# Kernel optimization log

Hardware: AMD Instinct MI355X
Metric: run time of the kernel (lower is better)

## Reference

```python
import jax, jax.numpy as jnp
import numpy as np

NH, HD, MB = 32, 64, 16        # heads, head_dim, TTT mini-batch size
BASE_LR = 1.0
ROPE_THETA = 10000.0


def _ln(x, w, b, eps):
    mu = x.mean(-1, keepdims=True)
    var = ((x - mu) ** 2).mean(-1, keepdims=True)
    return (x - mu) / jnp.sqrt(var + eps) * w + b


def _rotate_half(x):
    x1, x2 = jnp.split(x, 2, axis=-1)
    return jnp.concatenate([-x2, x1], axis=-1)


def _ln_l2_bwd(x, target, g, b, eps=1e-6):
    # grad of ||LN(x)*g+b - target||^2 / 2 wrt x (fused, as in ttt-lm)
    D = x.shape[-1]
    mu = x.mean(-1, keepdims=True)
    var = ((x - mu) ** 2).mean(-1, keepdims=True)
    std = jnp.sqrt(var + eps)
    xh = (x - mu) / std
    gxh = (g * xh + b - target) * g
    return (D * gxh - gxh.sum(-1, keepdims=True) - xh * (gxh * xh).sum(-1, keepdims=True)) / (D * std)


def _ttt_forward(x, q_w, k_w, v_w, o_w, ttt_lr_w, ttt_lr_b, token_idx_off,
                 ttt_norm_w, ttt_norm_b, W1, b1, post_w, post_b):
    B, L, C = x.shape
    NM = L // MB
    XQ = (x @ q_w).reshape(B, L, NH, HD).transpose(0, 2, 1, 3)  # [B,NH,L,HD]
    XK = (x @ k_w).reshape(B, L, NH, HD).transpose(0, 2, 1, 3)
    XV = (x @ v_w).reshape(B, L, NH, HD).transpose(0, 2, 1, 3)
    # rotary embedding at position_ids % mini_batch_size
    pos = (jnp.arange(L) % MB).astype(jnp.float32)
    inv = 1.0 / (ROPE_THETA ** (jnp.arange(0, HD, 2, dtype=jnp.float32) / HD))
    fr = pos[:, None] * inv[None, :]
    emb = jnp.concatenate([fr, fr], axis=-1)           # [L,HD]
    cos, sin = jnp.cos(emb), jnp.sin(emb)
    XQ = XQ * cos + _rotate_half(XQ) * sin
    XK = XK * cos + _rotate_half(XK) * sin
    # learning-rate gate (eta)
    Xm = x.reshape(B, NM, MB, C)
    ttt_lr = jax.nn.sigmoid(jnp.einsum('bnkc,hdc->bhnkd', Xm, ttt_lr_w)
                            + ttt_lr_b.reshape(1, NH, 1, 1, 1))       # [B,NH,NM,MB,1]
    ttt_lr_eta = BASE_LR * ttt_lr.transpose(0, 1, 2, 4, 3) / HD       # [B,NH,NM,1,MB]
    tok = jnp.maximum(1.0 / jnp.arange(1, MB + 1, dtype=jnp.float32) + token_idx_off, 0.0)
    eta = tok.reshape(1, 1, 1, MB, 1) * ttt_lr_eta                    # [B,NH,NM,MB,MB]

    def tomb(t):  # [B,NH,L,HD] -> [NM,B,NH,MB,HD]
        return t.reshape(B, NH, NM, MB, HD).transpose(2, 0, 1, 3, 4)

    xs = (tomb(XQ), tomb(XK), tomb(XV), eta.transpose(2, 0, 1, 3, 4))
    lw = ttt_norm_w.reshape(1, NH, 1, HD)
    lb = ttt_norm_b.reshape(1, NH, 1, HD)
    tril = jnp.tril(jnp.ones((MB, MB), x.dtype))
    W1s = jnp.broadcast_to(W1, (B, NH, HD, HD)).astype(x.dtype)
    b1s = jnp.broadcast_to(b1, (B, NH, 1, HD)).astype(x.dtype)

    def step(carry, xs_t):
        W1c, b1c = carry
        xq, xk, xv, et = xs_t                      # [B,NH,MB,HD], et [B,NH,MB,MB]
        Z1 = xk @ W1c + b1c
        grad = _ln_l2_bwd(Z1, xv - xk, lw, lb)     # grad of per-head TTT loss wrt Z1
        Attn1 = jnp.tril(xq @ xk.transpose(0, 1, 3, 2))
        b1_bar = b1c - (et * tril) @ grad
        Z1_bar = xq @ W1c - (et * Attn1) @ grad + b1_bar
        last_eta = et[:, :, -1, :, None]           # [B,NH,MB,1]
        W1n = W1c - jnp.einsum('bhki,bhkj->bhij', last_eta * xk, grad)
        b1n = b1c - (last_eta * grad).sum(-2, keepdims=True)
        out = xq + _ln(Z1_bar, lw, lb, 1e-6)
        return (W1n, b1n), out

    _, outs = jax.lax.scan(step, (W1s, b1s), xs)   # outs: [NM,B,NH,MB,HD]
    y = outs.transpose(1, 0, 3, 2, 4).reshape(B, L, C)
    y = _ln(y, post_w, post_b, 1e-6)
    return y @ o_w


def setup_inputs() -> dict:
    key = jax.random.key(0)
    ks = jax.random.split(key, 16)
    B, L, C, DH = 4, 2048, 2048, 1024
    s = 0.02
    return {
        'enc_input': jax.random.normal(ks[0], (B, L, C), jnp.float32),
        'ln1_w': jnp.ones((C,), jnp.float32), 'ln1_b': jnp.zeros((C,), jnp.float32),
        'q_w': jax.random.normal(ks[1], (C, C), jnp.float32) * s,
        'k_w': jax.random.normal(ks[2], (C, C), jnp.float32) * s,
        'v_w': jax.random.normal(ks[3], (C, C), jnp.float32) * s,
        'o_w': jax.random.normal(ks[4], (C, C), jnp.float32) * s,
        'ttt_lr_w': jax.random.normal(ks[5], (NH, 1, C), jnp.float32) * s,
        'ttt_lr_b': jax.random.normal(ks[6], (NH,), jnp.float32) * s,
        'token_idx_off': jax.random.normal(ks[7], (MB,), jnp.float32) * 0.01,
        'ttt_norm_w': jnp.ones((NH, HD), jnp.float32),
        'ttt_norm_b': jnp.zeros((NH, HD), jnp.float32),
        'W1': jax.random.normal(ks[8], (NH, HD, HD), jnp.float32) * s,
        'b1': jnp.zeros((NH, 1, HD), jnp.float32),
        'post_w': jnp.ones((C,), jnp.float32), 'post_b': jnp.zeros((C,), jnp.float32),
        'ffn_ln_w': jnp.ones((C,), jnp.float32), 'ffn_ln_b': jnp.zeros((C,), jnp.float32),
        'w1f': jax.random.normal(ks[9], (C, DH), jnp.float32) * s,
        'b1f': jnp.zeros((DH,), jnp.float32),
        'w2f': jax.random.normal(ks[10], (DH, C), jnp.float32) * s,
        'b2f': jnp.zeros((C,), jnp.float32),
    }


def reference(enc_input, ln1_w, ln1_b, q_w, k_w, v_w, o_w, ttt_lr_w, ttt_lr_b,
              token_idx_off, ttt_norm_w, ttt_norm_b, W1, b1, post_w, post_b,
              ffn_ln_w, ffn_ln_b, w1f, b1f, w2f, b2f):
    # pre-LN (torch default eps=1e-5) + TTT linear block + residual
    x = _ln(enc_input, ln1_w, ln1_b, 1e-5)
    y = _ttt_forward(x, q_w, k_w, v_w, o_w, ttt_lr_w, ttt_lr_b, token_idx_off,
                     ttt_norm_w, ttt_norm_b, W1, b1, post_w, post_b)
    y = y + enc_input
    # position-wise FFN (pre-LN eps=1e-6) + residual; dropout = eval no-op
    z = _ln(y, ffn_ln_w, ffn_ln_b, 1e-6)
    z = jax.nn.relu(z @ w1f + b1f) @ w2f + b2f
    return z + y
```

## Files before the change

### kernel.cpp

```cpp
#include <hip/hip_runtime.h>

typedef unsigned short u16;
typedef __attribute__((ext_vector_type(8))) short short8;
typedef __attribute__((ext_vector_type(8))) unsigned short ushort8;
typedef __attribute__((ext_vector_type(4))) float f32x4;
typedef __attribute__((ext_vector_type(2))) float f32x2;
typedef __attribute__((ext_vector_type(2))) unsigned int uint2v;

#define DEV __device__ __forceinline__

DEV float bf2f(u16 u){ union{unsigned int i; float f;} v; v.i = ((unsigned int)u)<<16u; return v.f; }
DEV u16 f2bf(float f){ union{float f; unsigned int i;} v; v.f=f; unsigned int r = v.i + 0x7FFFu + ((v.i>>16)&1u); return (u16)(r>>16); }

DEV void gload16(const u16* g, u16* l){
  __builtin_amdgcn_global_load_lds((const __attribute__((address_space(1))) void*)g,
                                   (__attribute__((address_space(3))) void*)l, 16, 0, 0);
}

DEV float wsum(float v){
  v += __shfl_xor(v, 32, 64);
  v += __shfl_xor(v, 16, 64);
  v += __shfl_xor(v, 8, 64);
  v += __shfl_xor(v, 4, 64);
  v += __shfl_xor(v, 2, 64);
  v += __shfl_xor(v, 1, 64);
  return v;
}

#if __has_builtin(__builtin_amdgcn_permlane16_swap) && __has_builtin(__builtin_amdgcn_permlane32_swap)
DEV float qsum(float v){
  unsigned u = __float_as_uint(v);
  uint2v a = __builtin_amdgcn_permlane16_swap(u, u, false, false);
  float s = __uint_as_float(a[0]) + __uint_as_float(a[1]);
  unsigned u2 = __float_as_uint(s);
  uint2v bsw = __builtin_amdgcn_permlane32_swap(u2, u2, false, false);
  return __uint_as_float(bsw[0]) + __uint_as_float(bsw[1]);
}
#else
DEV float qsum(float v){
  v += __shfl_xor(v, 16, 64);
  v += __shfl_xor(v, 32, 64);
  return v;
}
#endif

DEV float swap32(float v){ return __shfl_xor(v, 32, 64); }

DEV float block_sum(float v, float* red){
  v = wsum(v);
  __syncthreads();
  if((threadIdx.x & 63u)==0) red[threadIdx.x>>6] = v;
  __syncthreads();
  return red[0]+red[1]+red[2]+red[3];
}

#define BARS() do{ asm volatile("s_waitcnt lgkmcnt(0)" ::: "memory"); \
  __builtin_amdgcn_s_barrier(); __builtin_amdgcn_sched_barrier(0); }while(0)

__global__ __launch_bounds__(256) void ln_row(
    const float* __restrict__ in, const float* __restrict__ w, const float* __restrict__ bb,
    float eps, u16* __restrict__ outb)
{
  __shared__ float red[4];
  const int row = blockIdx.x, t = threadIdx.x;
  const float* p = in + (size_t)row*2048 + t*8;
  f32x4 a = *(const f32x4*)p;
  f32x4 c = *(const f32x4*)(p+4);
  float s = a[0]+a[1]+a[2]+a[3]+c[0]+c[1]+c[2]+c[3];
  s = block_sum(s, red);
  float mu = s*(1.f/2048.f);
  float vs = 0.f;
  #pragma unroll
  for(int j=0;j<4;j++){ float d=a[j]-mu; vs += d*d; }
  #pragma unroll
  for(int j=0;j<4;j++){ float d=c[j]-mu; vs += d*d; }
  vs = block_sum(vs, red);
  float rstd = rsqrtf(vs*(1.f/2048.f) + eps);
  f32x4 w0 = *(const f32x4*)(w + t*8);
  f32x4 w1 = *(const f32x4*)(w + t*8 + 4);
  f32x4 b0 = *(const f32x4*)(bb + t*8);
  f32x4 b1 = *(const f32x4*)(bb + t*8 + 4);
  ushort8 o;
  #pragma unroll
  for(int j=0;j<4;j++) o[j]   = f2bf((a[j]-mu)*rstd*w0[j] + b0[j]);
  #pragma unroll
  for(int j=0;j<4;j++) o[j+4] = f2bf((c[j]-mu)*rstd*w1[j] + b1[j]);
  *(ushort8*)(outb + (size_t)row*2048 + t*8) = o;
}

__global__ __launch_bounds__(256) void transpose_cast(
    const float* __restrict__ src, u16* __restrict__ dst, int K, int N)
{
  __shared__ float tile[32][33];
  const int kb = blockIdx.x*32, nb = blockIdx.y*32;
  const int tx = threadIdx.x & 31, ty = threadIdx.x >> 5;
  #pragma unroll
  for(int i=0;i<4;i++){
    int k = ty + i*8;
    tile[k][tx] = src[(size_t)(kb+k)*N + nb + tx];
  }
  __syncthreads();
  #pragma unroll
  for(int i=0;i<4;i++){
    int nn = ty + i*8;
    dst[(size_t)(nb+nn)*K + kb + tx] = f2bf(tile[tx][nn]);
  }
}

__global__ __launch_bounds__(256) void cast_lrw(const float* __restrict__ lrw, u16* __restrict__ dst)
{
  int i = blockIdx.x*256 + threadIdx.x;
  if (i < 32*2048) dst[i] = f2bf(lrw[i]);
  else dst[i] = 0;
}

__global__ void rope_init(const float* __restrict__ tio, float* __restrict__ cosb,
                          float* __restrict__ sinb, float* __restrict__ tokb)
{
  int t = blockIdx.x*256 + threadIdx.x;
  if (t < 1024){
// ... 119 lines not shown
          size_t idx = (size_t)(row0+rr)*Nld + col;
          float v = acc[mi][ni][rr];
          if (EPI==1 || EPI==3) v += resid[idx];
          if (EPI==2 || EPI==3) v += bias[col];
          if (EPI==2){ v = fmaxf(v, 0.f); Cb[idx] = f2bf(v); }
          else if (EPI==4){ Cb[idx] = f2bf(v); }
          else C[idx] = v;
        }
      }
    }
  }
}

#define W1LD 72
#define XLD  72
#define GTLD 40
#define EKLD 40
#define EALD 40
#define TD2  68

__global__ __launch_bounds__(512, 1) void ttt_scan(
    const u16* __restrict__ XQKV,
    const float* __restrict__ ropec, const float* __restrict__ ropes,
    const float* __restrict__ tokp,
    const float* __restrict__ nw, const float* __restrict__ nb,
    const float* __restrict__ lrb,
    const float* __restrict__ W1i,
    const float* __restrict__ b1i,
    float* __restrict__ Y)
{
  const int blk = blockIdx.x, b = blk>>5, h = blk&31;
  const int t = threadIdx.x, lane = t&63, wv = t>>6;
  const int fr = lane&15, quad = lane>>4;
  const int i0 = wv*2, i1 = i0+1;

  __shared__ u16 W1bf[2][64*W1LD];
  __shared__ u16 xqbf[2][16*XLD];
  __shared__ u16 xkbf[2][16*XLD];
  __shared__ u16 exkT[2][64*EKLD];
  __shared__ u16 gradTbf[2][64*GTLD];
  __shared__ u16 etaA[2][16*EALD];
  __shared__ float tgT2[2][16*TD2];
  __shared__ float xqT2[2][16*TD2];
  __shared__ float b1s[64];
  __shared__ float lrs[2][16];

  const float lrbh = lrb[h];
  const float cc0 = ropec[i0*64 + lane], ss0 = ropes[i0*64 + lane];
  const float cc1 = ropec[i1*64 + lane], ss1 = ropes[i1*64 + lane];
  const float ct = tokp[15]*(1.f/64.f);
  const float sg = (lane<32)? -1.f : 1.f;

  f32x2 lwr[16];
  #pragma unroll
  for(int m=0;m<4;m++)
    #pragma unroll
    for(int r=0;r<4;r++){
      int d = m*16+quad*4+r;
      lwr[m*4+r] = (f32x2){nw[h*64+d], nb[h*64+d]};
    }
  float tki[4];
  #pragma unroll
  for(int r=0;r<4;r++) tki[r] = tokp[quad*4+r];

  f32x4 wf0, wf1, wf2, wf3;
  if (wv < 4){
    const float* wsrc = W1i + (size_t)h*4096;
    #pragma unroll
    for(int r=0;r<4;r++){
      int d = wv*16+quad*4+r;
      wf0[r] = wsrc[( 0+fr)*64 + d];
      wf1[r] = wsrc[(16+fr)*64 + d];
      wf2[r] = wsrc[(32+fr)*64 + d];
      wf3[r] = wsrc[(48+fr)*64 + d];
    }
    #pragma unroll
    for(int r=0;r<4;r++){
      int d = wv*16+quad*4+r;
      W1bf[0][d*W1LD +  0 + fr] = f2bf(wf0[r]);
      W1bf[0][d*W1LD + 16 + fr] = f2bf(wf1[r]);
      W1bf[0][d*W1LD + 32 + fr] = f2bf(wf2[r]);
      W1bf[0][d*W1LD + 48 + fr] = f2bf(wf3[r]);
    }
  }
  for(int i=t;i<64*24;i+=512){
    int rr=i/24, cp=16+i%24;
    gradTbf[0][rr*GTLD+cp]=0; gradTbf[1][rr*GTLD+cp]=0;
    exkT[0][rr*EKLD+cp]=0;    exkT[1][rr*EKLD+cp]=0;
  }
  for(int i=t;i<16*24;i+=512){
    int rr=i/24, cp=16+i%24;
    etaA[0][rr*EALD+cp]=0; etaA[1][rr*EALD+cp]=0;
  }
  if (t<64) b1s[t]=b1i[h*64+t];

  auto stage = [&](int bf, u16 Pq0,u16 Pk0,u16 Pv0,u16 Pl0,
                           u16 Pq1,u16 Pk1,u16 Pv1,u16 Pl1){
    float q0=bf2f(Pq0), k0=bf2f(Pk0), v0=bf2f(Pv0);
    float q1=bf2f(Pq1), k1=bf2f(Pk1), v1=bf2f(Pv1);
    float qr0 = q0*cc0 + sg*swap32(q0)*ss0;
    float kr0 = k0*cc0 + sg*swap32(k0)*ss0;
    float qr1 = q1*cc1 + sg*swap32(q1)*ss1;
    float kr1 = k1*cc1 + sg*swap32(k1)*ss1;
    float lr0 = 1.f/(1.f + expf(-(bf2f(Pl0) + lrbh)));
    float lr1 = 1.f/(1.f + expf(-(bf2f(Pl1) + lrbh)));
    xqbf[bf][i0*XLD+lane] = f2bf(qr0);
    xqbf[bf][i1*XLD+lane] = f2bf(qr1);
    xkbf[bf][i0*XLD+lane] = f2bf(kr0);
    xkbf[bf][i1*XLD+lane] = f2bf(kr1);
    exkT[bf][lane*EKLD+i0] = f2bf(-ct*lr0*kr0);
    exkT[bf][lane*EKLD+i1] = f2bf(-ct*lr1*kr1);
    tgT2[bf][i0*TD2+lane] = v0 - kr0;
    tgT2[bf][i1*TD2+lane] = v1 - kr1;
    xqT2[bf][i0*TD2+lane] = qr0;
    xqT2[bf][i1*TD2+lane] = qr1;
    if (lane==0){ lrs[bf][i0]=lr0; lrs[bf][i1]=lr1; }
  };

  {
    const size_t rb = (size_t)b*2048;
    const u16* p0 = XQKV + (rb+i0)*6272 + h*64 + lane;
    const u16* p1 = XQKV + (rb+i1)*6272 + h*64 + lane;
    u16 l0 = XQKV[(rb+i0)*6272 + 6144 + h];
    u16 l1 = XQKV[(rb+i1)*6272 + 6144 + h];
    stage(0, p0[0],p0[2048],p0[4096],l0, p1[0],p1[2048],p1[4096],l1);
  }
  __syncthreads();

  const f32x4 fzero = (f32x4){0.f,0.f,0.f,0.f};

  f32x4 zqP0=fzero, zqP1=fzero, zqP2=fzero, zqP3=fzero;
  f32x4 b1qP0=fzero, b1qP1=fzero, b1qP2=fzero, b1qP3=fzero;

  auto do_out = [&](int pbuf, size_t rb){
    short8 be = *(const short8*)&etaA[pbuf][fr*EALD + quad*8];
    f32x4 c20,c21,c22,c23;
    c20 = __builtin_amdgcn_mfma_f32_16x16x32_bf16(*(const short8*)&gradTbf[pbuf][( 0+fr)*GTLD + quad*8], be, fzero, 0,0,0);
    c21 = __builtin_amdgcn_mfma_f32_16x16x32_bf16(*(const short8*)&gradTbf[pbuf][(16+fr)*GTLD + quad*8], be, fzero, 0,0,0);
    c22 = __builtin_amdgcn_mfma_f32_16x16x32_bf16(*(const short8*)&gradTbf[pbuf][(32+fr)*GTLD + quad*8], be, fzero, 0,0,0);
    c23 = __builtin_amdgcn_mfma_f32_16x16x32_bf16(*(const short8*)&gradTbf[pbuf][(48+fr)*GTLD + quad*8], be, fzero, 0,0,0);
    f32x4 xqv0 = *(const f32x4*)&xqT2[pbuf][fr*TD2 +  0 + quad*4];
    f32x4 xqv1 = *(const f32x4*)&xqT2[pbuf][fr*TD2 + 16 + quad*4];
    f32x4 xqv2 = *(const f32x4*)&xqT2[pbuf][fr*TD2 + 32 + quad*4];
    f32x4 xqv3 = *(const f32x4*)&xqT2[pbuf][fr*TD2 + 48 + quad*4];
    f32x4 zb0,zb1,zb2,zb3;
    float s1=0.f, s2=0.f;
    #pragma unroll
    for(int r=0;r<4;r++){
      zb0[r] = zqP0[r] + b1qP0[r] + c20[r];
      zb1[r] = zqP1[r] + b1qP1[r] + c21[r];
      zb2[r] = zqP2[r] + b1qP2[r] + c22[r];
      zb3[r] = zqP3[r] + b1qP3[r] + c23[r];
      s1 += zb0[r]+zb1[r]+zb2[r]+zb3[r];
      s2 += zb0[r]*zb0[r]+zb1[r]*zb1[r]+zb2[r]*zb2[r]+zb3[r]*zb3[r];
    }
    s1 = qsum(s1); s2 = qsum(s2);
    float mu = s1*(1.f/64.f);
    float var = s2*(1.f/64.f) - mu*mu;
    float rstd = rsqrtf(var + 1e-6f);
    #pragma unroll
    for(int m=0;m<4;m++){
      f32x4* zp = (m==0)?&zb0:(m==1)?&zb1:(m==2)?&zb2:&zb3;
      const f32x4* xp = (m==0)?&xqv0:(m==1)?&xqv1:(m==2)?&xqv2:&xqv3;
      f32x4 o;
      #pragma unroll
      for(int r=0;r<4;r++){
        f32x2 wb = lwr[m*4+r];
        float xh = ((*zp)[r] - mu)*rstd;
        o[r] = (*xp)[r] + xh*wb[0] + wb[1];
      }
      *(f32x4*)&Y[(rb+fr)*2048 + h*64 + m*16 + quad*4] = o;
    }
  };

  for(int n=0;n<128;n++){
    const int cur = n&1, nxt = cur^1, pb = cur^1;
    const int cb = cur, nbuf = cur^1;
    const size_t rbase = (size_t)b*2048 + n*16;

    u16 Pq0=0,Pk0=0,Pv0=0,Pl0=0,Pq1=0,Pk1=0,Pv1=0,Pl1=0;
    if (n<127){
      const size_t rb2 = rbase + 16;
      const u16* p0 = XQKV + (rb2+i0)*6272 + h*64 + lane;
      const u16* p1 = XQKV + (rb2+i1)*6272 + h*64 + lane;
      Pq0=p0[0]; Pk0=p0[2048]; Pv0=p0[4096];
      Pq1=p1[0]; Pk1=p1[2048]; Pv1=p1[4096];
      Pl0=XQKV[(rb2+i0)*6272 + 6144 + h];
      Pl1=XQKV[(rb2+i1)*6272 + 6144 + h];
    }

    if (wv < 2){
      f32x4 b1v0 = *(const f32x4*)&b1s[ 0+quad*4];
      f32x4 b1v1 = *(const f32x4*)&b1s[16+quad*4];
      f32x4 b1v2 = *(const f32x4*)&b1s[32+quad*4];
      f32x4 b1v3 = *(const f32x4*)&b1s[48+quad*4];
      f32x4 tgv0 = *(const f32x4*)&tgT2[cur][fr*TD2 +  0 + quad*4];
      f32x4 tgv1 = *(const f32x4*)&tgT2[cur][fr*TD2 + 16 + quad*4];
      f32x4 tgv2 = *(const f32x4*)&tgT2[cur][fr*TD2 + 32 + quad*4];
      f32x4 tgv3 = *(const f32x4*)&tgT2[cur][fr*TD2 + 48 + quad*4];
      short8 bk0 = *(const short8*)&xkbf[cur][fr*XLD + quad*8];
      short8 bk1 = *(const short8*)&xkbf[cur][fr*XLD + 32 + quad*8];
      f32x4 z0,z1,z2,z3;
      z0 = __builtin_amdgcn_mfma_f32_16x16x32_bf16(*(const short8*)&W1bf[cb][( 0+fr)*W1LD + quad*8],      bk0, fzero, 0,0,0);
      z0 = __builtin_amdgcn_mfma_f32_16x16x32_bf16(*(const short8*)&W1bf[cb][( 0+fr)*W1LD + 32 + quad*8], bk1, z0,    0,0,0);
      z1 = __builtin_amdgcn_mfma_f32_16x16x32_bf16(*(const short8*)&W1bf[cb][(16+fr)*W1LD + quad*8],      bk0, fzero, 0,0,0);
      z1 = __builtin_amdgcn_mfma_f32_16x16x32_bf16(*(const short8*)&W1bf[cb][(16+fr)*W1LD + 32 + quad*8], bk1, z1,    0,0,0);
      z2 = __builtin_amdgcn_mfma_f32_16x16x32_bf16(*(const short8*)&W1bf[cb][(32+fr)*W1LD + quad*8],      bk0, fzero, 0,0,0);
      z2 = __builtin_amdgcn_mfma_f32_16x16x32_bf16(*(const short8*)&W1bf[cb][(32+fr)*W1LD + 32 + quad*8], bk1, z2,    0,0,0);
      z3 = __builtin_amdgcn_mfma_f32_16x16x32_bf16(*(const short8*)&W1bf[cb][(48+fr)*W1LD + quad*8],      bk0, fzero, 0,0,0);
      z3 = __builtin_amdgcn_mfma_f32_16x16x32_bf16(*(const short8*)&W1bf[cb][(48+fr)*W1LD + 32 + quad*8], bk1, z3,    0,0,0);
      f32x4 xh0,xh1,xh2,xh3;
      {
        float s1=0.f, s2=0.f;
        #pragma unroll
        for(int r=0;r<4;r++){
          z0[r] += b1v0[r];
          z1[r] += b1v1[r];
          z2[r] += b1v2[r];
          z3[r] += b1v3[r];
          s1 += z0[r]+z1[r]+z2[r]+z3[r];
          s2 += z0[r]*z0[r]+z1[r]*z1[r]+z2[r]*z2[r]+z3[r]*z3[r];
        }
        s1 = qsum(s1); s2 = qsum(s2);
        float mu = s1*(1.f/64.f);
        float var = s2*(1.f/64.f) - mu*mu;
        float rstd = rsqrtf(var + 1e-6f);
        float u1=0.f, u2=0.f;
        #pragma unroll
        for(int m=0;m<4;m++){
          f32x4* zp = (m==0)?&z0:(m==1)?&z1:(m==2)?&z2:&z3;
          f32x4* xp = (m==0)?&xh0:(m==1)?&xh1:(m==2)?&xh2:&xh3;
          const f32x4* tp = (m==0)?&tgv0:(m==1)?&tgv1:(m==2)?&tgv2:&tgv3;
          #pragma unroll
          for(int r=0;r<4;r++){
            f32x2 wb = lwr[m*4+r];
            float xh = ((*zp)[r] - mu)*rstd;
            float gx = (wb[0]*xh + wb[1] - (*tp)[r])*wb[0];
            (*xp)[r] = xh;
            (*zp)[r] = gx;
            u1 += gx; u2 += gx*xh;
          }
        }
        u1 = qsum(u1); u2 = qsum(u2);
        const float c64 = rstd*(1.f/64.f);
        #pragma unroll
        for(int m=0;m<4;m++){
          f32x4* zp = (m==0)?&z0:(m==1)?&z1:(m==2)?&z2:&z3;
          f32x4* xp = (m==0)?&xh0:(m==1)?&xh1:(m==2)?&xh2:&xh3;
          #pragma unroll
          for(int r=0;r<4;r++)
            (*zp)[r] = (64.f*(*zp)[r] - u1 - (*xp)[r]*u2)*c64;
        }
      }
      f32x4 zA = (wv==0)? z0 : z2;
      f32x4 zB = (wv==0)? z1 : z3;
      const int rb0 = wv*32;
      #pragma unroll
      for(int r=0;r<4;r++){
        gradTbf[cur][(rb0+quad*4+r)*GTLD + fr]    = f2bf(zA[r]);
        gradTbf[cur][(rb0+16+quad*4+r)*GTLD + fr] = f2bf(zB[r]);
      }
    }
    else if (wv == 4){
      short8 bq0 = *(const short8*)&xqbf[cur][fr*XLD + quad*8];
      short8 bq1 = *(const short8*)&xqbf[cur][fr*XLD + 32 + quad*8];
      f32x4 zqN0,zqN1,zqN2,zqN3;
      zqN0 = __builtin_amdgcn_mfma_f32_16x16x32_bf16(*(const short8*)&W1bf[cb][( 0+fr)*W1LD + quad*8],      bq0, fzero, 0,0,0);
      zqN0 = __builtin_amdgcn_mfma_f32_16x16x32_bf16(*(const short8*)&W1bf[cb][( 0+fr)*W1LD + 32 + quad*8], bq1, zqN0,  0,0,0);
      zqN1 = __builtin_amdgcn_mfma_f32_16x16x32_bf16(*(const short8*)&W1bf[cb][(16+fr)*W1LD + quad*8],      bq0, fzero, 0,0,0);
      zqN1 = __builtin_amdgcn_mfma_f32_16x16x32_bf16(*(const short8*)&W1bf[cb][(16+fr)*W1LD + 32 + quad*8], bq1, zqN1,  0,0,0);
      zqN2 = __builtin_amdgcn_mfma_f32_16x16x32_bf16(*(const short8*)&W1bf[cb][(32+fr)*W1LD + quad*8],      bq0, fzero, 0,0,0);
      zqN2 = __builtin_amdgcn_mfma_f32_16x16x32_bf16(*(const short8*)&W1bf[cb][(32+fr)*W1LD + 32 + quad*8], bq1, zqN2,  0,0,0);
      zqN3 = __builtin_amdgcn_mfma_f32_16x16x32_bf16(*(const short8*)&W1bf[cb][(48+fr)*W1LD + quad*8],      bq0, fzero, 0,0,0);
      zqN3 = __builtin_amdgcn_mfma_f32_16x16x32_bf16(*(const short8*)&W1bf[cb][(48+fr)*W1LD + 32 + quad*8], bq1, zqN3,  0,0,0);
      if (n > 0) do_out(pb, rbase - 16);
      zqP0=zqN0; zqP1=zqN1; zqP2=zqN2; zqP3=zqN3;
      b1qP0 = *(const f32x4*)&b1s[ 0+quad*4];
      b1qP1 = *(const f32x4*)&b1s[16+quad*4];
      b1qP2 = *(const f32x4*)&b1s[32+quad*4];
      b1qP3 = *(const f32x4*)&b1s[48+quad*4];
    }
    else if (wv == 7){
      short8 aq0 = *(const short8*)&xqbf[cur][fr*XLD + quad*8];
      short8 aq1 = *(const short8*)&xqbf[cur][fr*XLD + 32 + quad*8];
      short8 bk0 = *(const short8*)&xkbf[cur][fr*XLD + quad*8];
      short8 bk1 = *(const short8*)&xkbf[cur][fr*XLD + 32 + quad*8];
      f32x4 at;
      at = __builtin_amdgcn_mfma_f32_16x16x32_bf16(aq0, bk0, fzero, 0,0,0);
      at = __builtin_amdgcn_mfma_f32_16x16x32_bf16(aq1, bk1, at,    0,0,0);
      float lrj = lrs[cur][fr]*(1.f/64.f);
      #pragma unroll
      for(int r=0;r<4;r++){
        int i = quad*4 + r;
        float val = (fr <= i) ? -tki[r]*lrj*(1.f + at[r]) : 0.f;
        etaA[cur][i*EALD + fr] = f2bf(val);
      }
    }
    BARS();

    if (wv < 4){
      short8 ga = *(const short8*)&gradTbf[cur][(wv*16+fr)*GTLD + quad*8];
      short8 e0 = *(const short8*)&exkT[cur][( 0+fr)*EKLD + quad*8];
      short8 e1 = *(const short8*)&exkT[cur][(16+fr)*EKLD + quad*8];
      short8 e2 = *(const short8*)&exkT[cur][(32+fr)*EKLD + quad*8];
      short8 e3 = *(const short8*)&exkT[cur][(48+fr)*EKLD + quad*8];
      wf0 = __builtin_amdgcn_mfma_f32_16x16x32_bf16(ga, e0, wf0, 0,0,0);
      wf1 = __builtin_amdgcn_mfma_f32_16x16x32_bf16(ga, e1, wf1, 0,0,0);
      wf2 = __builtin_amdgcn_mfma_f32_16x16x32_bf16(ga, e2, wf2, 0,0,0);
      wf3 = __builtin_amdgcn_mfma_f32_16x16x32_bf16(ga, e3, wf3, 0,0,0);
      #pragma unroll
      for(int r=0;r<4;r++){
        int d = wv*16+quad*4+r;
        W1bf[nbuf][d*W1LD +  0 + fr] = f2bf(wf0[r]);
        W1bf[nbuf][d*W1LD + 16 + fr] = f2bf(wf1[r]);
        W1bf[nbuf][d*W1LD + 32 + fr] = f2bf(wf2[r]);
        W1bf[nbuf][d*W1LD + 48 + fr] = f2bf(wf3[r]);
      }
    }
    else if (wv == 5){
      const int d = lane;
      short8 g0 = *(const short8*)&gradTbf[cur][d*GTLD + 0];
      short8 g1 = *(const short8*)&gradTbf[cur][d*GTLD + 8];
      float s = 0.f;
      #pragma unroll
      for(int j=0;j<8;j++) s += lrs[cur][j]   * bf2f((u16)g0[j]);
      #pragma unroll
      for(int j=0;j<8;j++) s += lrs[cur][8+j] * bf2f((u16)g1[j]);
      b1s[d] -= ct * s;
    }
    if (n<127) stage(nxt, Pq0,Pk0,Pv0,Pl0, Pq1,Pk1,Pv1,Pl1);
    BARS();
  }

  if (wv == 4) do_out(1, (size_t)b*2048 + 127*16);
}

extern "C" void kernel_launch(void* const* d_in, const int* in_sizes, int n_in,
                              void* d_out, int out_size, void* d_ws, size_t ws_size,
                              hipStream_t stream)
{
  const float* enc   = (const float*)d_in[0];
  const float* ln1w  = (const float*)d_in[1];
  const float* ln1b  = (const float*)d_in[2];
  const float* qw    = (const float*)d_in[3];
  const float* kw    = (const float*)d_in[4];
  const float* vw    = (const float*)d_in[5];
  const float* ow    = (const float*)d_in[6];
  const float* lrw   = (const float*)d_in[7];
  const float* lrb   = (const float*)d_in[8];
  const float* tio   = (const float*)d_in[9];
  const float* tnw   = (const float*)d_in[10];
  const float* tnb   = (const float*)d_in[11];
  const float* W1i   = (const float*)d_in[12];
  const float* b1i   = (const float*)d_in[13];
  const float* postw = (const float*)d_in[14];
  const float* postb = (const float*)d_in[15];
  const float* flnw  = (const float*)d_in[16];
  const float* flnb  = (const float*)d_in[17];
  const float* w1f   = (const float*)d_in[18];
  const float* b1f   = (const float*)d_in[19];
  const float* w2f   = (const float*)d_in[20];
  const float* b2f   = (const float*)d_in[21];
  float* out = (float*)d_out;

  char* ws = (char*)d_ws;
  size_t off = 0;
  auto alloc = [&](size_t bytes)->void*{ void* p = ws + off; off += (bytes + 255) & ~(size_t)255; return p; };
  u16*   regA  = (u16*)  alloc(8192ull*2048*2);
  u16*   wqkvT = (u16*)  alloc(6400ull*2048*2);
  u16*   XQKV  = (u16*)  alloc(8192ull*6272*2);
  float* yb    = (float*)alloc(8192ull*2048*4);
  float* ropec = (float*)alloc(1024*4);
  float* ropes = (float*)alloc(1024*4);
  float* tokb  = (float*)alloc(64*4);

  u16* oT   = wqkvT;
  u16* w1fT = wqkvT + 2048ull*2048;
  u16* w2fT = w1fT + 1024ull*2048;
  u16* hbf  = XQKV;
  float* y2 = yb;

  static bool s_attr = false;
  if (!s_attr){
    s_attr = true;
    (void)hipFuncSetAttribute(reinterpret_cast<const void*>(gemm256<4>), hipFuncAttributeMaxDynamicSharedMemorySize, 131072);
    (void)hipFuncSetAttribute(reinterpret_cast<const void*>(gemm256<1>), hipFuncAttributeMaxDynamicSharedMemorySize, 131072);
    (void)hipFuncSetAttribute(reinterpret_cast<const void*>(gemm256<2>), hipFuncAttributeMaxDynamicSharedMemorySize, 131072);
    (void)hipFuncSetAttribute(reinterpret_cast<const void*>(gemm256<3>), hipFuncAttributeMaxDynamicSharedMemorySize, 131072);
  }

  rope_init<<<4, 256, 0, stream>>>(tio, ropec, ropes, tokb);

  dim3 tg1(64, 64);
  transpose_cast<<<tg1, 256, 0, stream>>>(qw, wqkvT,               2048, 2048);
  transpose_cast<<<tg1, 256, 0, stream>>>(kw, wqkvT + 2048ull*2048, 2048, 2048);
  transpose_cast<<<tg1, 256, 0, stream>>>(vw, wqkvT + 4096ull*2048, 2048, 2048);
  cast_lrw<<<2048, 256, 0, stream>>>(lrw, wqkvT + 6144ull*2048);

  ln_row<<<8192, 256, 0, stream>>>(enc, ln1w, ln1b, 1e-5f, regA);

  gemm256<4><<<32*25, 512, 131072, stream>>>(regA, wqkvT, nullptr, XQKV,
                                             nullptr, nullptr, 6272, 6272, 2048, 25);

  transpose_cast<<<tg1, 256, 0, stream>>>(ow, oT, 2048, 2048);
  dim3 tg2(64, 32);
  transpose_cast<<<tg2, 256, 0, stream>>>(w1f, w1fT, 2048, 1024);
  dim3 tg3(32, 64);
  transpose_cast<<<tg3, 256, 0, stream>>>(w2f, w2fT, 1024, 2048);

  ttt_scan<<<128, 512, 0, stream>>>(XQKV, ropec, ropes, tokb, tnw, tnb, lrb, W1i, b1i, yb);

  ln_row<<<8192, 256, 0, stream>>>(yb, postw, postb, 1e-6f, regA);
  gemm256<1><<<32*8, 512, 131072, stream>>>(regA, oT, y2, nullptr,
                                            nullptr, enc, 2048, 2048, 2048, 8);

  ln_row<<<8192, 256, 0, stream>>>(y2, flnw, flnb, 1e-6f, regA);
  gemm256<2><<<32*4, 512, 131072, stream>>>(regA, w1fT, nullptr, hbf,
                                            b1f, nullptr, 1024, 1024, 2048, 4);
  gemm256<3><<<32*8, 512, 131072, stream>>>(hbf, w2fT, out, nullptr,
                                            b2f, y2, 2048, 2048, 1024, 8);
}
```

Baseline: 800.7 us.

## Move TTT staging to dedicated waves with triple buffering; use one wave per row in LayerNorm

The scan kernel now hands input staging (RoPE, sigmoid gate, LDS writes) to four otherwise idle waves. These waves prefetch two mini-batches ahead into triple-buffered LDS slots while the compute waves run the current step. This takes staging and global loads off the serial critical path between barriers, at the cost of more LDS and some work moved between waves (the b1 update goes to wave 7, the W1 update to the stager waves). Separately, LayerNorm is rewritten to use one wavefront per row, so the block-level barrier reductions become wave shuffles and the grid shrinks to a quarter.

```diff
diff --git a/kernel.cpp b/kernel.cpp
--- a/kernel.cpp
+++ b/kernel.cpp
@@ -3,6 +3,7 @@
 typedef unsigned short u16;
 typedef __attribute__((ext_vector_type(8))) short short8;
 typedef __attribute__((ext_vector_type(8))) unsigned short ushort8;
+typedef __attribute__((ext_vector_type(4))) unsigned short us4;
 typedef __attribute__((ext_vector_type(4))) float f32x4;
 typedef __attribute__((ext_vector_type(2))) float f32x2;
 typedef __attribute__((ext_vector_type(2))) unsigned int uint2v;
@@ -46,14 +47,6 @@
 
 DEV float swap32(float v){ return __shfl_xor(v, 32, 64); }
 
-DEV float block_sum(float v, float* red){
-  v = wsum(v);
-  __syncthreads();
-  if((threadIdx.x & 63u)==0) red[threadIdx.x>>6] = v;
-  __syncthreads();
-  return red[0]+red[1]+red[2]+red[3];
-}
-
 #define BARS() do{ asm volatile("s_waitcnt lgkmcnt(0)" ::: "memory"); \
   __builtin_amdgcn_s_barrier(); __builtin_amdgcn_sched_barrier(0); }while(0)
 
@@ -61,31 +54,33 @@
     const float* __restrict__ in, const float* __restrict__ w, const float* __restrict__ bb,
     float eps, u16* __restrict__ outb)
 {
-  __shared__ float red[4];
-  const int row = blockIdx.x, t = threadIdx.x;
-  const float* p = in + (size_t)row*2048 + t*8;
-  f32x4 a = *(const f32x4*)p;
-  f32x4 c = *(const f32x4*)(p+4);
-  float s = a[0]+a[1]+a[2]+a[3]+c[0]+c[1]+c[2]+c[3];
-  s = block_sum(s, red);
+  const int wv = threadIdx.x>>6, lane = threadIdx.x&63;
+  const int row = blockIdx.x*4 + wv;
+  const float* p = in + (size_t)row*2048 + lane*4;
+  f32x4 a[8];
+  #pragma unroll
+  for(int j=0;j<8;j++) a[j] = *(const f32x4*)(p + j*256);
+  float s = 0.f;
+  #pragma unroll
+  for(int j=0;j<8;j++) s += a[j][0]+a[j][1]+a[j][2]+a[j][3];
+  s = wsum(s);
   float mu = s*(1.f/2048.f);
   float vs = 0.f;
   #pragma unroll
-  for(int j=0;j<4;j++){ float d=a[j]-mu; vs += d*d; }
-  #pragma unroll
-  for(int j=0;j<4;j++){ float d=c[j]-mu; vs += d*d; }
-  vs = block_sum(vs, red);
+  for(int j=0;j<8;j++)
+    #pragma unroll
+    for(int r=0;r<4;r++){ float d=a[j][r]-mu; vs += d*d; }
+  vs = wsum(vs);
   float rstd = rsqrtf(vs*(1.f/2048.f) + eps);
-  f32x4 w0 = *(const f32x4*)(w + t*8);
-  f32x4 w1 = *(const f32x4*)(w + t*8 + 4);
-  f32x4 b0 = *(const f32x4*)(bb + t*8);
-  f32x4 b1 = *(const f32x4*)(bb + t*8 + 4);
-  ushort8 o;
-  #pragma unroll
-  for(int j=0;j<4;j++) o[j]   = f2bf((a[j]-mu)*rstd*w0[j] + b0[j]);
-  #pragma unroll
-  for(int j=0;j<4;j++) o[j+4] = f2bf((c[j]-mu)*rstd*w1[j] + b1[j]);
-  *(ushort8*)(outb + (size_t)row*2048 + t*8) = o;
+  #pragma unroll
+  for(int j=0;j<8;j++){
+    f32x4 wj = *(const f32x4*)(w  + j*256 + lane*4);
+    f32x4 bj = *(const f32x4*)(bb + j*256 + lane*4);
+    us4 o;
+    #pragma unroll
+    for(int r=0;r<4;r++) o[r] = f2bf((a[j][r]-mu)*rstd*wj[r] + bj[r]);
+    *(us4*)(outb + (size_t)row*2048 + j*256 + lane*4) = o;
+  }
 }
 
 __global__ __launch_bounds__(256) void transpose_cast(
@@ -271,22 +266,21 @@
   const int blk = blockIdx.x, b = blk>>5, h = blk&31;
   const int t = threadIdx.x, lane = t&63, wv = t>>6;
   const int fr = lane&15, quad = lane>>4;
-  const int i0 = wv*2, i1 = i0+1;
+  const bool isStager = (wv==2)||(wv==3)||(wv==5)||(wv==6);
+  const int sm = (wv>=5)? wv-3 : wv-2;
 
   __shared__ u16 W1bf[2][64*W1LD];
-  __shared__ u16 xqbf[2][16*XLD];
-  __shared__ u16 xkbf[2][16*XLD];
-  __shared__ u16 exkT[2][64*EKLD];
+  __shared__ u16 xqbf[3][16*XLD];
+  __shared__ u16 xkbf[3][16*XLD];
+  __shared__ u16 exkT[3][64*EKLD];
   __shared__ u16 gradTbf[2][64*GTLD];
   __shared__ u16 etaA[2][16*EALD];
-  __shared__ float tgT2[2][16*TD2];
-  __shared__ float xqT2[2][16*TD2];
+  __shared__ float tgT2[3][16*TD2];
+  __shared__ float xqT2[3][16*TD2];
   __shared__ float b1s[64];
-  __shared__ float lrs[2][16];
+  __shared__ float lrs[3][16];
 
   const float lrbh = lrb[h];
-  const float cc0 = ropec[i0*64 + lane], ss0 = ropes[i0*64 + lane];
-  const float cc1 = ropec[i1*64 + lane], ss1 = ropes[i1*64 + lane];
   const float ct = tokp[15]*(1.f/64.f);
   const float sg = (lane<32)? -1.f : 1.f;
 
@@ -302,12 +296,19 @@
   #pragma unroll
   for(int r=0;r<4;r++) tki[r] = tokp[quad*4+r];
 
+  float ccj[4], ssj[4];
   f32x4 wf0, wf1, wf2, wf3;
-  if (wv < 4){
+  u16 Pq[4], Pk[4], Pv[4], Pl[4];
+  if (isStager){
+    #pragma unroll
+    for(int j=0;j<4;j++){
+      ccj[j] = ropec[(sm*4+j)*64 + lane];
+      ssj[j] = ropes[(sm*4+j)*64 + lane];
+    }
     const float* wsrc = W1i + (size_t)h*4096;
     #pragma unroll
     for(int r=0;r<4;r++){
-      int d = wv*16+quad*4+r;
+      int d = sm*16+quad*4+r;
       wf0[r] = wsrc[( 0+fr)*64 + d];
       wf1[r] = wsrc[(16+fr)*64 + d];
       wf2[r] = wsrc[(32+fr)*64 + d];
@@ -315,7 +316,7 @@
     }
     #pragma unroll
     for(int r=0;r<4;r++){
-      int d = wv*16+quad*4+r;
+      int d = sm*16+quad*4+r;
       W1bf[0][d*W1LD +  0 + fr] = f2bf(wf0[r]);
       W1bf[0][d*W1LD + 16 + fr] = f2bf(wf1[r]);
       W1bf[0][d*W1LD + 32 + fr] = f2bf(wf2[r]);
@@ -325,7 +326,7 @@
   for(int i=t;i<64*24;i+=512){
     int rr=i/24, cp=16+i%24;
     gradTbf[0][rr*GTLD+cp]=0; gradTbf[1][rr*GTLD+cp]=0;
-    exkT[0][rr*EKLD+cp]=0;    exkT[1][rr*EKLD+cp]=0;
+    exkT[0][rr*EKLD+cp]=0; exkT[1][rr*EKLD+cp]=0; exkT[2][rr*EKLD+cp]=0;
   }
   for(int i=t;i<16*24;i+=512){
     int rr=i/24, cp=16+i%24;
@@ -333,36 +334,36 @@
   }
   if (t<64) b1s[t]=b1i[h*64+t];
 
-  auto stage = [&](int bf, u16 Pq0,u16 Pk0,u16 Pv0,u16 Pl0,
-                           u16 Pq1,u16 Pk1,u16 Pv1,u16 Pl1){
-    float q0=bf2f(Pq0), k0=bf2f(Pk0), v0=bf2f(Pv0);
-    float q1=bf2f(Pq1), k1=bf2f(Pk1), v1=bf2f(Pv1);
-    float qr0 = q0*cc0 + sg*swap32(q0)*ss0;
-    float kr0 = k0*cc0 + sg*swap32(k0)*ss0;
-    float qr1 = q1*cc1 + sg*swap32(q1)*ss1;
-    float kr1 = k1*cc1 + sg*swap32(k1)*ss1;
-    float lr0 = 1.f/(1.f + expf(-(bf2f(Pl0) + lrbh)));
-    float lr1 = 1.f/(1.f + expf(-(bf2f(Pl1) + lrbh)));
-    xqbf[bf][i0*XLD+lane] = f2bf(qr0);
-    xqbf[bf][i1*XLD+lane] = f2bf(qr1);
-    xkbf[bf][i0*XLD+lane] = f2bf(kr0);
-    xkbf[bf][i1*XLD+lane] = f2bf(kr1);
-    exkT[bf][lane*EKLD+i0] = f2bf(-ct*lr0*kr0);
-    exkT[bf][lane*EKLD+i1] = f2bf(-ct*lr1*kr1);
-    tgT2[bf][i0*TD2+lane] = v0 - kr0;
-    tgT2[bf][i1*TD2+lane] = v1 - kr1;
-    xqT2[bf][i0*TD2+lane] = qr0;
-    xqT2[bf][i1*TD2+lane] = qr1;
-    if (lane==0){ lrs[bf][i0]=lr0; lrs[bf][i1]=lr1; }
+  auto loadP = [&](int n){
+    const size_t rb = (size_t)b*2048 + n*16;
+    #pragma unroll
+    for(int j=0;j<4;j++){
+      const u16* p = XQKV + (rb+sm*4+j)*6272 + h*64 + lane;
+      Pq[j]=p[0]; Pk[j]=p[2048]; Pv[j]=p[4096];
+      Pl[j]=XQKV[(rb+sm*4+j)*6272 + 6144 + h];
+    }
   };
-
-  {
-    const size_t rb = (size_t)b*2048;
-    const u16* p0 = XQKV + (rb+i0)*6272 + h*64 + lane;
-    const u16* p1 = XQKV + (rb+i1)*6272 + h*64 + lane;
-    u16 l0 = XQKV[(rb+i0)*6272 + 6144 + h];
-    u16 l1 = XQKV[(rb+i1)*6272 + 6144 + h];
-    stage(0, p0[0],p0[2048],p0[4096],l0, p1[0],p1[2048],p1[4096],l1);
+  auto stage4 = [&](int slot){
+    #pragma unroll
+    for(int j=0;j<4;j++){
+      const int i = sm*4+j;
+      float q=bf2f(Pq[j]), k=bf2f(Pk[j]), v=bf2f(Pv[j]);
+      float qr = q*ccj[j] + sg*swap32(q)*ssj[j];
+      float kr = k*ccj[j] + sg*swap32(k)*ssj[j];
+      float lr = 1.f/(1.f + expf(-(bf2f(Pl[j]) + lrbh)));
+      xqbf[slot][i*XLD+lane] = f2bf(qr);
+      xkbf[slot][i*XLD+lane] = f2bf(kr);
+      exkT[slot][lane*EKLD+i] = f2bf(-ct*lr*kr);
+      tgT2[slot][i*TD2+lane] = v - kr;
+      xqT2[slot][i*TD2+lane] = qr;
+      if (lane==0) lrs[slot][i]=lr;
+    }
+  };
+
+  if (isStager){
+    loadP(0);
+    stage4(0);
+    loadP(1);
   }
   __syncthreads();
 
@@ -371,17 +372,17 @@
   f32x4 zqP0=fzero, zqP1=fzero, zqP2=fzero, zqP3=fzero;
   f32x4 b1qP0=fzero, b1qP1=fzero, b1qP2=fzero, b1qP3=fzero;
 
-  auto do_out = [&](int pbuf, size_t rb){
-    short8 be = *(const short8*)&etaA[pbuf][fr*EALD + quad*8];
+  auto do_out = [&](int p2, int p3, size_t rb){
+    short8 be = *(const short8*)&etaA[p2][fr*EALD + quad*8];
     f32x4 c20,c21,c22,c23;
-    c20 = __builtin_amdgcn_mfma_f32_16x16x32_bf16(*(const short8*)&gradTbf[pbuf][( 0+fr)*GTLD + quad*8], be, fzero, 0,0,0);
-    c21 = __builtin_amdgcn_mfma_f32_16x16x32_bf16(*(const short8*)&gradTbf[pbuf][(16+fr)*GTLD + quad*8], be, fzero, 0,0,0);
-    c22 = __builtin_amdgcn_mfma_f32_16x16x32_bf16(*(const short8*)&gradTbf[pbuf][(32+fr)*GTLD + quad*8], be, fzero, 0,0,0);
-    c23 = __builtin_amdgcn_mfma_f32_16x16x32_bf16(*(const short8*)&gradTbf[pbuf][(48+fr)*GTLD + quad*8], be, fzero, 0,0,0);
-    f32x4 xqv0 = *(const f32x4*)&xqT2[pbuf][fr*TD2 +  0 + quad*4];
-    f32x4 xqv1 = *(const f32x4*)&xqT2[pbuf][fr*TD2 + 16 + quad*4];
-    f32x4 xqv2 = *(const f32x4*)&xqT2[pbuf][fr*TD2 + 32 + quad*4];
-    f32x4 xqv3 = *(const f32x4*)&xqT2[pbuf][fr*TD2 + 48 + quad*4];
+    c20 = __builtin_amdgcn_mfma_f32_16x16x32_bf16(*(const short8*)&gradTbf[p2][( 0+fr)*GTLD + quad*8], be, fzero, 0,0,0);
+    c21 = __builtin_amdgcn_mfma_f32_16x16x32_bf16(*(const short8*)&gradTbf[p2][(16+fr)*GTLD + quad*8], be, fzero, 0,0,0);
+    c22 = __builtin_amdgcn_mfma_f32_16x16x32_bf16(*(const short8*)&gradTbf[p2][(32+fr)*GTLD + quad*8], be, fzero, 0,0,0);
+    c23 = __builtin_amdgcn_mfma_f32_16x16x32_bf16(*(const short8*)&gradTbf[p2][(48+fr)*GTLD + quad*8], be, fzero, 0,0,0);
+    f32x4 xqv0 = *(const f32x4*)&xqT2[p3][fr*TD2 +  0 + quad*4];
+    f32x4 xqv1 = *(const f32x4*)&xqT2[p3][fr*TD2 + 16 + quad*4];
+    f32x4 xqv2 = *(const f32x4*)&xqT2[p3][fr*TD2 + 32 + quad*4];
+    f32x4 xqv3 = *(const f32x4*)&xqT2[p3][fr*TD2 + 48 + quad*4];
     f32x4 zb0,zb1,zb2,zb3;
     float s1=0.f, s2=0.f;
     #pragma unroll
@@ -412,42 +413,34 @@
     }
   };
 
+  int c3 = 0;
   for(int n=0;n<128;n++){
-    const int cur = n&1, nxt = cur^1, pb = cur^1;
-    const int cb = cur, nbuf = cur^1;
+    const int cur2 = n&1, pb2 = cur2^1;
+    const int cur3 = c3;
+    const int nxt3 = (c3==2)? 0 : c3+1;
+    const int pb3  = (c3==0)? 2 : c3-1;
     const size_t rbase = (size_t)b*2048 + n*16;
-
-    u16 Pq0=0,Pk0=0,Pv0=0,Pl0=0,Pq1=0,Pk1=0,Pv1=0,Pl1=0;
-    if (n<127){
-      const size_t rb2 = rbase + 16;
-      const u16* p0 = XQKV + (rb2+i0)*6272 + h*64 + lane;
-      const u16* p1 = XQKV + (rb2+i1)*6272 + h*64 + lane;
-      Pq0=p0[0]; Pk0=p0[2048]; Pv0=p0[4096];
-      Pq1=p1[0]; Pk1=p1[2048]; Pv1=p1[4096];
-      Pl0=XQKV[(rb2+i0)*6272 + 6144 + h];
-      Pl1=XQKV[(rb2+i1)*6272 + 6144 + h];
-    }
 
     if (wv < 2){
       f32x4 b1v0 = *(const f32x4*)&b1s[ 0+quad*4];
       f32x4 b1v1 = *(const f32x4*)&b1s[16+quad*4];
       f32x4 b1v2 = *(const f32x4*)&b1s[32+quad*4];
       f32x4 b1v3 = *(const f32x4*)&b1s[48+quad*4];
-      f32x4 tgv0 = *(const f32x4*)&tgT2[cur][fr*TD2 +  0 + quad*4];
-      f32x4 tgv1 = *(const f32x4*)&tgT2[cur][fr*TD2 + 16 + quad*4];
-      f32x4 tgv2 = *(const f32x4*)&tgT2[cur][fr*TD2 + 32 + quad*4];
-      f32x4 tgv3 = *(const f32x4*)&tgT2[cur][fr*TD2 + 48 + quad*4];
-      short8 bk0 = *(const short8*)&xkbf[cur][fr*XLD + quad*8];
-      short8 bk1 = *(const short8*)&xkbf[cur][fr*XLD + 32 + quad*8];
+      f32x4 tgv0 = *(const f32x4*)&tgT2[cur3][fr*TD2 +  0 + quad*4];
+      f32x4 tgv1 = *(const f32x4*)&tgT2[cur3][fr*TD2 + 16 + quad*4];
+      f32x4 tgv2 = *(const f32x4*)&tgT2[cur3][fr*TD2 + 32 + quad*4];
+      f32x4 tgv3 = *(const f32x4*)&tgT2[cur3][fr*TD2 + 48 + quad*4];
+      short8 bk0 = *(const short8*)&xkbf[cur3][fr*XLD + quad*8];
+      short8 bk1 = *(const short8*)&xkbf[cur3][fr*XLD + 32 + quad*8];
       f32x4 z0,z1,z2,z3;
-      z0 = __builtin_amdgcn_mfma_f32_16x16x32_bf16(*(const short8*)&W1bf[cb][( 0+fr)*W1LD + quad*8],      bk0, fzero, 0,0,0);
-      z0 = __builtin_amdgcn_mfma_f32_16x16x32_bf16(*(const short8*)&W1bf[cb][( 0+fr)*W1LD + 32 + quad*8], bk1, z0,    0,0,0);
-      z1 = __builtin_amdgcn_mfma_f32_16x16x32_bf16(*(const short8*)&W1bf[cb][(16+fr)*W1LD + quad*8],      bk0, fzero, 0,0,0);
-      z1 = __builtin_amdgcn_mfma_f32_16x16x32_bf16(*(const short8*)&W1bf[cb][(16+fr)*W1LD + 32 + quad*8], bk1, z1,    0,0,0);
-      z2 = __builtin_amdgcn_mfma_f32_16x16x32_bf16(*(const short8*)&W1bf[cb][(32+fr)*W1LD + quad*8],      bk0, fzero, 0,0,0);
-      z2 = __builtin_amdgcn_mfma_f32_16x16x32_bf16(*(const short8*)&W1bf[cb][(32+fr)*W1LD + 32 + quad*8], bk1, z2,    0,0,0);
-      z3 = __builtin_amdgcn_mfma_f32_16x16x32_bf16(*(const short8*)&W1bf[cb][(48+fr)*W1LD + quad*8],      bk0, fzero, 0,0,0);
-      z3 = __builtin_amdgcn_mfma_f32_16x16x32_bf16(*(const short8*)&W1bf[cb][(48+fr)*W1LD + 32 + quad*8], bk1, z3,    0,0,0);
+      z0 = __builtin_amdgcn_mfma_f32_16x16x32_bf16(*(const short8*)&W1bf[cur2][( 0+fr)*W1LD + quad*8],      bk0, fzero, 0,0,0);
+      z0 = __builtin_amdgcn_mfma_f32_16x16x32_bf16(*(const short8*)&W1bf[cur2][( 0+fr)*W1LD + 32 + quad*8], bk1, z0,    0,0,0);
+      z1 = __builtin_amdgcn_mfma_f32_16x16x32_bf16(*(const short8*)&W1bf[cur2][(16+fr)*W1LD + quad*8],      bk0, fzero, 0,0,0);
+      z1 = __builtin_amdgcn_mfma_f32_16x16x32_bf16(*(const short8*)&W1bf[cur2][(16+fr)*W1LD + 32 + quad*8], bk1, z1,    0,0,0);
+      z2 = __builtin_amdgcn_mfma_f32_16x16x32_bf16(*(const short8*)&W1bf[cur2][(32+fr)*W1LD + quad*8],      bk0, fzero, 0,0,0);
+      z2 = __builtin_amdgcn_mfma_f32_16x16x32_bf16(*(const short8*)&W1bf[cur2][(32+fr)*W1LD + 32 + quad*8], bk1, z2,    0,0,0);
+      z3 = __builtin_amdgcn_mfma_f32_16x16x32_bf16(*(const short8*)&W1bf[cur2][(48+fr)*W1LD + quad*8],      bk0, fzero, 0,0,0);
+      z3 = __builtin_amdgcn_mfma_f32_16x16x32_bf16(*(const short8*)&W1bf[cur2][(48+fr)*W1LD + 32 + quad*8], bk1, z3,    0,0,0);
       f32x4 xh0,xh1,xh2,xh3;
       {
         float s1=0.f, s2=0.f;
@@ -496,23 +489,23 @@
       const int rb0 = wv*32;
       #pragma unroll
       for(int r=0;r<4;r++){
-        gradTbf[cur][(rb0+quad*4+r)*GTLD + fr]    = f2bf(zA[r]);
-        gradTbf[cur][(rb0+16+quad*4+r)*GTLD + fr] = f2bf(zB[r]);
+        gradTbf[cur2][(rb0+quad*4+r)*GTLD + fr]    = f2bf(zA[r]);
+        gradTbf[cur2][(rb0+16+quad*4+r)*GTLD + fr] = f2bf(zB[r]);
       }
     }
     else if (wv == 4){
-      short8 bq0 = *(const short8*)&xqbf[cur][fr*XLD + quad*8];
-      short8 bq1 = *(const short8*)&xqbf[cur][fr*XLD + 32 + quad*8];
+      short8 bq0 = *(const short8*)&xqbf[cur3][fr*XLD + quad*8];
+      short8 bq1 = *(const short8*)&xqbf[cur3][fr*XLD + 32 + quad*8];
       f32x4 zqN0,zqN1,zqN2,zqN3;
-      zqN0 = __builtin_amdgcn_mfma_f32_16x16x32_bf16(*(const short8*)&W1bf[cb][( 0+fr)*W1LD + quad*8],      bq0, fzero, 0,0,0);
-      zqN0 = __builtin_amdgcn_mfma_f32_16x16x32_bf16(*(const short8*)&W1bf[cb][( 0+fr)*W1LD + 32 + quad*8], bq1, zqN0,  0,0,0);
-      zqN1 = __builtin_amdgcn_mfma_f32_16x16x32_bf16(*(const short8*)&W1bf[cb][(16+fr)*W1LD + quad*8],      bq0, fzero, 0,0,0);
-      zqN1 = __builtin_amdgcn_mfma_f32_16x16x32_bf16(*(const short8*)&W1bf[cb][(16+fr)*W1LD + 32 + quad*8], bq1, zqN1,  0,0,0);
-      zqN2 = __builtin_amdgcn_mfma_f32_16x16x32_bf16(*(const short8*)&W1bf[cb][(32+fr)*W1LD + quad*8],      bq0, fzero, 0,0,0);
-      zqN2 = __builtin_amdgcn_mfma_f32_16x16x32_bf16(*(const short8*)&W1bf[cb][(32+fr)*W1LD + 32 + quad*8], bq1, zqN2,  0,0,0);
-      zqN3 = __builtin_amdgcn_mfma_f32_16x16x32_bf16(*(const short8*)&W1bf[cb][(48+fr)*W1LD + quad*8],      bq0, fzero, 0,0,0);
-      zqN3 = __builtin_amdgcn_mfma_f32_16x16x32_bf16(*(const short8*)&W1bf[cb][(48+fr)*W1LD + 32 + quad*8], bq1, zqN3,  0,0,0);
-      if (n > 0) do_out(pb, rbase - 16);
+      zqN0 = __builtin_amdgcn_mfma_f32_16x16x32_bf16(*(const short8*)&W1bf[cur2][( 0+fr)*W1LD + quad*8],      bq0, fzero, 0,0,0);
+      zqN0 = __builtin_amdgcn_mfma_f32_16x16x32_bf16(*(const short8*)&W1bf[cur2][( 0+fr)*W1LD + 32 + quad*8], bq1, zqN0,  0,0,0);
+      zqN1 = __builtin_amdgcn_mfma_f32_16x16x32_bf16(*(const short8*)&W1bf[cur2][(16+fr)*W1LD + quad*8],      bq0, fzero, 0,0,0);
+      zqN1 = __builtin_amdgcn_mfma_f32_16x16x32_bf16(*(const short8*)&W1bf[cur2][(16+fr)*W1LD + 32 + quad*8], bq1, zqN1,  0,0,0);
+      zqN2 = __builtin_amdgcn_mfma_f32_16x16x32_bf16(*(const short8*)&W1bf[cur2][(32+fr)*W1LD + quad*8],      bq0, fzero, 0,0,0);
+      zqN2 = __builtin_amdgcn_mfma_f32_16x16x32_bf16(*(const short8*)&W1bf[cur2][(32+fr)*W1LD + 32 + quad*8], bq1, zqN2,  0,0,0);
+      zqN3 = __builtin_amdgcn_mfma_f32_16x16x32_bf16(*(const short8*)&W1bf[cur2][(48+fr)*W1LD + quad*8],      bq0, fzero, 0,0,0);
+      zqN3 = __builtin_amdgcn_mfma_f32_16x16x32_bf16(*(const short8*)&W1bf[cur2][(48+fr)*W1LD + 32 + quad*8], bq1, zqN3,  0,0,0);
+      if (n > 0) do_out(pb2, pb3, rbase - 16);
       zqP0=zqN0; zqP1=zqN1; zqP2=zqN2; zqP3=zqN3;
       b1qP0 = *(const f32x4*)&b1s[ 0+quad*4];
       b1qP1 = *(const f32x4*)&b1s[16+quad*4];
@@ -520,58 +513,62 @@
       b1qP3 = *(const f32x4*)&b1s[48+quad*4];
     }
     else if (wv == 7){
-      short8 aq0 = *(const short8*)&xqbf[cur][fr*XLD + quad*8];
-      short8 aq1 = *(const short8*)&xqbf[cur][fr*XLD + 32 + quad*8];
-      short8 bk0 = *(const short8*)&xkbf[cur][fr*XLD + quad*8];
-      short8 bk1 = *(const short8*)&xkbf[cur][fr*XLD + 32 + quad*8];
+      short8 aq0 = *(const short8*)&xqbf[cur3][fr*XLD + quad*8];
+      short8 aq1 = *(const short8*)&xqbf[cur3][fr*XLD + 32 + quad*8];
+      short8 bk0 = *(const short8*)&xkbf[cur3][fr*XLD + quad*8];
+      short8 bk1 = *(const short8*)&xkbf[cur3][fr*XLD + 32 + quad*8];
       f32x4 at;
       at = __builtin_amdgcn_mfma_f32_16x16x32_bf16(aq0, bk0, fzero, 0,0,0);
       at = __builtin_amdgcn_mfma_f32_16x16x32_bf16(aq1, bk1, at,    0,0,0);
-      float lrj = lrs[cur][fr]*(1.f/64.f);
+      float lrj = lrs[cur3][fr]*(1.f/64.f);
       #pragma unroll
       for(int r=0;r<4;r++){
         int i = quad*4 + r;
         float val = (fr <= i) ? -tki[r]*lrj*(1.f + at[r]) : 0.f;
-        etaA[cur][i*EALD + fr] = f2bf(val);
+        etaA[cur2][i*EALD + fr] = f2bf(val);
       }
     }
+    else {
+      if (n < 127) stage4(nxt3);
+      if (n < 126) loadP(n+2);
+    }
     BARS();
 
-    if (wv < 4){
-      short8 ga = *(const short8*)&gradTbf[cur][(wv*16+fr)*GTLD + quad*8];
-      short8 e0 = *(const short8*)&exkT[cur][( 0+fr)*EKLD + quad*8];
-      short8 e1 = *(const short8*)&exkT[cur][(16+fr)*EKLD + quad*8];
-      short8 e2 = *(const short8*)&exkT[cur][(32+fr)*EKLD + quad*8];
-      short8 e3 = *(const short8*)&exkT[cur][(48+fr)*EKLD + quad*8];
+    if (isStager){
+      short8 ga = *(const short8*)&gradTbf[cur2][(sm*16+fr)*GTLD + quad*8];
+      short8 e0 = *(const short8*)&exkT[cur3][( 0+fr)*EKLD + quad*8];
+      short8 e1 = *(const short8*)&exkT[cur3][(16+fr)*EKLD + quad*8];
+      short8 e2 = *(const short8*)&exkT[cur3][(32+fr)*EKLD + quad*8];
+      short8 e3 = *(const short8*)&exkT[cur3][(48+fr)*EKLD + quad*8];
       wf0 = __builtin_amdgcn_mfma_f32_16x16x32_bf16(ga, e0, wf0, 0,0,0);
       wf1 = __builtin_amdgcn_mfma_f32_16x16x32_bf16(ga, e1, wf1, 0,0,0);
       wf2 = __builtin_amdgcn_mfma_f32_16x16x32_bf16(ga, e2, wf2, 0,0,0);
       wf3 = __builtin_amdgcn_mfma_f32_16x16x32_bf16(ga, e3, wf3, 0,0,0);
       #pragma unroll
       for(int r=0;r<4;r++){
-        int d = wv*16+quad*4+r;
-        W1bf[nbuf][d*W1LD +  0 + fr] = f2bf(wf0[r]);
-        W1bf[nbuf][d*W1LD + 16 + fr] = f2bf(wf1[r]);
-        W1bf[nbuf][d*W1LD + 32 + fr] = f2bf(wf2[r]);
-        W1bf[nbuf][d*W1LD + 48 + fr] = f2bf(wf3[r]);
+        int d = sm*16+quad*4+r;
+        W1bf[pb2][d*W1LD +  0 + fr] = f2bf(wf0[r]);
+        W1bf[pb2][d*W1LD + 16 + fr] = f2bf(wf1[r]);
+        W1bf[pb2][d*W1LD + 32 + fr] = f2bf(wf2[r]);
+        W1bf[pb2][d*W1LD + 48 + fr] = f2bf(wf3[r]);
       }
     }
-    else if (wv == 5){
+    else if (wv == 7){
       const int d = lane;
-      short8 g0 = *(const short8*)&gradTbf[cur][d*GTLD + 0];
-      short8 g1 = *(const short8*)&gradTbf[cur][d*GTLD + 8];
+      short8 g0 = *(const short8*)&gradTbf[cur2][d*GTLD + 0];
+      short8 g1 = *(const short8*)&gradTbf[cur2][d*GTLD + 8];
       float s = 0.f;
       #pragma unroll
-      for(int j=0;j<8;j++) s += lrs[cur][j]   * bf2f((u16)g0[j]);
+      for(int j=0;j<8;j++) s += lrs[cur3][j]   * bf2f((u16)g0[j]);
       #pragma unroll
-      for(int j=0;j<8;j++) s += lrs[cur][8+j] * bf2f((u16)g1[j]);
+      for(int j=0;j<8;j++) s += lrs[cur3][8+j] * bf2f((u16)g1[j]);
       b1s[d] -= ct * s;
     }
-    if (n<127) stage(nxt, Pq0,Pk0,Pv0,Pl0, Pq1,Pk1,Pv1,Pl1);
     BARS();
-  }
-
-  if (wv == 4) do_out(1, (size_t)b*2048 + 127*16);
+    c3 = nxt3;
+  }
+
+  if (wv == 4) do_out(1, 1, (size_t)b*2048 + 127*16);
 }
 
 extern "C" void kernel_launch(void* const* d_in, const int* in_sizes, int n_in,
@@ -636,7 +633,7 @@
   transpose_cast<<<tg1, 256, 0, stream>>>(vw, wqkvT + 4096ull*2048, 2048, 2048);
   cast_lrw<<<2048, 256, 0, stream>>>(lrw, wqkvT + 6144ull*2048);
 
-  ln_row<<<8192, 256, 0, stream>>>(enc, ln1w, ln1b, 1e-5f, regA);
+  ln_row<<<2048, 256, 0, stream>>>(enc, ln1w, ln1b, 1e-5f, regA);
 
   gemm256<4><<<32*25, 512, 131072, stream>>>(regA, wqkvT, nullptr, XQKV,
                                              nullptr, nullptr, 6272, 6272, 2048, 25);
@@ -649,11 +646,11 @@
 
   ttt_scan<<<128, 512, 0, stream>>>(XQKV, ropec, ropes, tokb, tnw, tnb, lrb, W1i, b1i, yb);
 
-  ln_row<<<8192, 256, 0, stream>>>(yb, postw, postb, 1e-6f, regA);
+  ln_row<<<2048, 256, 0, stream>>>(yb, postw, postb, 1e-6f, regA);
   gemm256<1><<<32*8, 512, 131072, stream>>>(regA, oT, y2, nullptr,
                                             nullptr, enc, 2048, 2048, 2048, 8);
 
-  ln_row<<<8192, 256, 0, stream>>>(y2, flnw, flnb, 1e-6f, regA);
+  ln_row<<<2048, 256, 0, stream>>>(y2, flnw, flnb, 1e-6f, regA);
   gemm256<2><<<32*4, 512, 131072, stream>>>(regA, w1fT, nullptr, hbf,
                                             b1f, nullptr, 1024, 1024, 2048, 4);
   gemm256<3><<<32*8, 512, 131072, stream>>>(hbf, w2fT, out, nullptr,
```

After: 768.6 us. 1.04x faster.
